# Kernel tuning notes

Hardware: AMD Instinct MI355X
Metric: run time of the kernel (lower is better)

Reference implementation:

```python
import jax, jax.numpy as jnp
import numpy as np
from jax import lax

B, C, H, W = 8, 256, 32, 32
HEADS = 8
NUM_OFF = 9
OFF_SCALE = 0.1


def setup_inputs() -> dict:
    key = jax.random.key(0)
    ks = jax.random.split(key, 8)
    f = lambda k, s, sc: jax.random.normal(k, s, dtype=jnp.float32) * sc
    return {
        'query_map': f(ks[0], (B, C, H, W), 1.0),
        'kv_map': f(ks[1], (B, C, H, W), 1.0),
        'Wq': f(ks[2], (C, C), C ** -0.5),
        'Wk': f(ks[3], (C, C), C ** -0.5),
        'Wv': f(ks[4], (C, C), C ** -0.5),
        'Woff1': f(ks[5], (C // 2, C, 3, 3), (C * 9) ** -0.5),
        'boff1': jnp.zeros((C // 2,), jnp.float32),
        'Woff2': f(ks[6], (NUM_OFF * 2, C // 2), (C // 2) ** -0.5),
        'boff2': jnp.zeros((NUM_OFF * 2,), jnp.float32),
        'Wout': f(ks[7], (C, C), C ** -0.5),
        'bout': jnp.zeros((C,), jnp.float32),
    }


def grid_sample_bilinear_border(img, grid):
    """img: (B,C,H,W); grid: (B,H,W,2) with (x,y) in [-1,1], align_corners=True,
    padding_mode='border'. Returns (B,C,H,W)."""
    Bn, Cn, Hn, Wn = img.shape
    x = (grid[..., 0] + 1.0) * 0.5 * (Wn - 1)
    y = (grid[..., 1] + 1.0) * 0.5 * (Hn - 1)
    # border padding: clamp continuous coords into the valid range
    x = jnp.clip(x, 0.0, Wn - 1)
    y = jnp.clip(y, 0.0, Hn - 1)
    x0 = jnp.floor(x)
    y0 = jnp.floor(y)
    wx = x - x0
    wy = y - y0
    x0i = x0.astype(jnp.int32)
    y0i = y0.astype(jnp.int32)
    x1i = jnp.minimum(x0i + 1, Wn - 1)
    y1i = jnp.minimum(y0i + 1, Hn - 1)
    flat = img.reshape(Bn, Cn, Hn * Wn)

    def gat(iy, ix):
        idx = (iy * Wn + ix).reshape(Bn, 1, -1)  # broadcasts over channels
        return jnp.take_along_axis(flat, idx, axis=2)

    v00 = gat(y0i, x0i)
    v01 = gat(y0i, x1i)
    v10 = gat(y1i, x0i)
    v11 = gat(y1i, x1i)
    wxf = wx.reshape(Bn, 1, -1)
    wyf = wy.reshape(Bn, 1, -1)
    out = (v00 * (1 - wxf) + v01 * wxf) * (1 - wyf) + (v10 * (1 - wxf) + v11 * wxf) * wyf
    return out.reshape(Bn, Cn, Hn, Wn)


def reference(query_map, kv_map, Wq, Wk, Wv, Woff1, boff1, Woff2, boff2, Wout, bout):
    Bn, Cn, Hn, Wn = query_map.shape
    hd = Cn // HEADS
    # 1x1 conv projections as channel einsums
    q = jnp.einsum('oc,bchw->bohw', Wq, query_map)
    # offset network: 3x3 conv -> relu -> 1x1 conv
    h1 = lax.conv_general_dilated(q, Woff1, (1, 1), 'SAME',
                                  dimension_numbers=('NCHW', 'OIHW', 'NCHW'))
    h1 = jax.nn.relu(h1 + boff1[None, :, None, None])
    offsets = jnp.einsum('oc,bchw->bohw', Woff2, h1) + boff2[None, :, None, None]
    offsets = offsets.reshape(Bn, NUM_OFF, 2, Hn, Wn)
    offset = offsets[:, 0] * OFF_SCALE  # (B,2,H,W); ch0 -> x, ch1 -> y
    # normalized base grid in [-1,1] (align_corners=True convention)
    gx = jnp.linspace(-1.0, 1.0, Wn, dtype=q.dtype)[None, :]  # (1,W)
    gy = jnp.linspace(-1.0, 1.0, Hn, dtype=q.dtype)[:, None]  # (H,1)
    vx = gx[None] + offset[:, 0]  # (B,H,W)
    vy = gy[None] + offset[:, 1]
    vgrid = jnp.stack([vx, vy], axis=-1)  # (B,H,W,2)
    kv_sampled = grid_sample_bilinear_border(kv_map, vgrid)
    k = jnp.einsum('oc,bchw->bohw', Wk, kv_sampled)
    v = jnp.einsum('oc,bchw->bohw', Wv, kv_sampled)
    # (B,C,H,W) -> (B,heads,HW,hd)
    def to_heads(t):
        return t.reshape(Bn, HEADS, hd, Hn * Wn).transpose(0, 1, 3, 2)
    qh, kh, vh = to_heads(q), to_heads(k), to_heads(v)
    scale = hd ** -0.5
    attn = jnp.einsum('bhqd,bhkd->bhqk', qh, kh) * scale
    attn = jax.nn.softmax(attn, axis=-1)
    out = jnp.einsum('bhqk,bhkd->bhqd', attn, vh)
    out = out.transpose(0, 1, 3, 2).reshape(Bn, Cn, Hn, Wn)
    out = jnp.einsum('oc,bchw->bohw', Wout, out) + bout[None, :, None, None]
    return out
```

## Files before the change

### kernel.cpp

```cpp
#include <hip/hip_runtime.h>

#define HW_ 1024

typedef __attribute__((ext_vector_type(8))) short bf16x8;
typedef __attribute__((ext_vector_type(4))) short bf16x4;
typedef __attribute__((ext_vector_type(4))) float f32x4;

__device__ inline unsigned short f2bf(float f) {
  unsigned int u = __float_as_uint(f);
  u += 0x7FFF + ((u >> 16) & 1);
  return (unsigned short)(u >> 16);
}
__device__ inline unsigned short f2bf_fast(float f) {
  return (unsigned short)((__float_as_uint(f) + 0x8000u) >> 16);
}
__device__ inline float bf2f(unsigned short h) {
  return __uint_as_float(((unsigned int)h) << 16);
}
__device__ inline void async_copy16(const void* g, void* l) {
  __builtin_amdgcn_global_load_lds(
      (const __attribute__((address_space(1))) unsigned int*)g,
      (__attribute__((address_space(3))) unsigned int*)l, 16, 0, 0);
}

__global__ __launch_bounds__(256) void fused0(
    const float* __restrict__ kv,
    const float* __restrict__ Wq, const float* __restrict__ Wk,
    const float* __restrict__ Wv, const float* __restrict__ Wo,
    const float* __restrict__ Woff1, const float* __restrict__ Xf,
    short* __restrict__ WH, short* __restrict__ WL, short* __restrict__ wb,
    float* __restrict__ kvT,
    short* __restrict__ Yt, short* __restrict__ Yh2, short* __restrict__ Yl2)
{
  __shared__ float T[256][33];
  __shared__ short Bsh[32][40];
  __shared__ short Bsl[32][40];
  const int bid = blockIdx.x, t = threadIdx.x;

  if (bid < 512) {
    const int w    = t >> 6;
    const int lane = t & 63;
    const int ln   = lane & 15;
    const int qd   = lane >> 4;
    const int bp0  = (bid & 255) * 32;
    const int om   = (bid >> 8) * 128 + w * 32;
    const int bB   = bp0 >> 10, p0l = bp0 & 1023;

    f32x4 acc[2][2] = {};
#pragma unroll
    for (int k0 = 0; k0 < 256; k0 += 32) {
      __syncthreads();
      {
        int pp = t & 31, cg = t >> 5;
        float fv[4];
#pragma unroll
        for (int j = 0; j < 4; ++j)
          fv[j] = Xf[((size_t)(bB * 256 + k0 + cg * 4 + j)) * HW_ + p0l + pp];
        bf16x4 h4, l4;
#pragma unroll
        for (int j = 0; j < 4; ++j) {
          unsigned short h = f2bf(fv[j]);
          h4[j] = (short)h;
          l4[j] = (short)f2bf(fv[j] - bf2f(h));
        }
        *(bf16x4*)&Bsh[pp][cg * 4] = h4;
        *(bf16x4*)&Bsl[pp][cg * 4] = l4;
      }
      __syncthreads();

      bf16x8 Ah[2], Al[2], Bh[2], Bl[2];
#pragma unroll
      for (int mt = 0; mt < 2; ++mt) {
        const float* ws = &Wq[((size_t)(om + mt * 16 + ln)) * 256 + k0 + qd * 8];
        float4 fa = *(const float4*)ws;
        float4 fb = *(const float4*)(ws + 4);
        float f8[8] = {fa.x, fa.y, fa.z, fa.w, fb.x, fb.y, fb.z, fb.w};
#pragma unroll
        for (int j = 0; j < 8; ++j) {
          unsigned short h = f2bf(f8[j]);
          Ah[mt][j] = (short)h;
          Al[mt][j] = (short)f2bf(f8[j] - bf2f(h));
        }
      }
#pragma unroll
      for (int nt = 0; nt < 2; ++nt) {
        Bh[nt] = *(const bf16x8*)&Bsh[nt * 16 + ln][qd * 8];
        Bl[nt] = *(const bf16x8*)&Bsl[nt * 16 + ln][qd * 8];
      }
#pragma unroll
      for (int mt = 0; mt < 2; ++mt)
#pragma unroll
        for (int nt = 0; nt < 2; ++nt) {
          acc[mt][nt] = __builtin_amdgcn_mfma_f32_16x16x32_bf16(Ah[mt], Bh[nt], acc[mt][nt], 0, 0, 0);
          acc[mt][nt] = __builtin_amdgcn_mfma_f32_16x16x32_bf16(Ah[mt], Bl[nt], acc[mt][nt], 0, 0, 0);
          acc[mt][nt] = __builtin_amdgcn_mfma_f32_16x16x32_bf16(Al[mt], Bh[nt], acc[mt][nt], 0, 0, 0);
        }
    }

    const float sc = 0.25506063286f;
#pragma unroll
    for (int mt = 0; mt < 2; ++mt)
#pragma unroll
      for (int nt = 0; nt < 2; ++nt) {
        int bp = bp0 + nt * 16 + ln;
        int b = bp >> 10, p = bp & 1023;
#pragma unroll
        for (int i = 0; i < 4; ++i) {
          int o = om + mt * 16 + qd * 4 + i;
          int h = o >> 5, d = o & 31;
          Yt[(((size_t)(b * 8 + h)) * 1024 + p) * 32 + d] = (short)f2bf(acc[mt][nt][i] * sc);
        }
        int ob = om + mt * 16 + qd * 4;
        bf16x4 h4, l4;
#pragma unroll
        for (int i = 0; i < 4; ++i) {
          float f = acc[mt][nt][i];
          unsigned short h = f2bf(f);
          h4[i] = (short)h;
          l4[i] = (short)f2bf(f - bf2f(h));
        }
        *(bf16x4*)&Yh2[(size_t)bp * 256 + ob] = h4;
        *(bf16x4*)&Yl2[(size_t)bp * 256 + ob] = l4;
      }

  } else if (bid < 768) {
    int tb = bid - 512;
    int b = tb >> 5, p0 = (tb & 31) * 32;
    int pp = t & 31, cg = t >> 5;
#pragma unroll
    for (int i = 0; i < 32; ++i) {
      int c = cg * 32 + i;
      T[c][pp] = kv[((size_t)(b * 256 + c)) * HW_ + p0 + pp];
    }
    __syncthreads();
#pragma unroll
    for (int r = 0; r < 8; ++r) {
      int e = t + 256 * r;
      int c4 = (e & 63) * 4, pp2 = e >> 6;
      float4 v4;
      v4.x = T[c4 + 0][pp2];
      v4.y = T[c4 + 1][pp2];
      v4.z = T[c4 + 2][pp2];
      v4.w = T[c4 + 3][pp2];
      *(float4*)&kvT[((size_t)(b * 1024 + p0 + pp2)) * 256 + c4] = v4;
    }
  } else if (bid < 960) {
    int b2 = bid - 768;
    int mat = b2 >> 6;
    int loc = (b2 & 63) * 1024 + t * 4;
    const float* W = (mat == 0) ? Wk : (mat == 1) ? Wv : Wo;
    float4 f4 = *(const float4*)&W[loc];
    float f[4] = {f4.x, f4.y, f4.z, f4.w};
    bf16x4 h4, l4;
#pragma unroll
    for (int j = 0; j < 4; ++j) {
      unsigned short h = f2bf(f[j]);
      h4[j] = (short)h;
      l4[j] = (short)f2bf(f[j] - bf2f(h));
    }
    *(bf16x4*)&WH[(mat + 1) * 65536 + loc] = h4;
    *(bf16x4*)&WL[(mat + 1) * 65536 + loc] = l4;
  } else {
    int e0 = (bid - 960) * 1024 + t * 4;
#pragma unroll
    for (int j = 0; j < 4; ++j) {
      int e = e0 + j;
      int c = e & 255;
      int o = (e >> 8) & 127;
      int tap = e >> 15;
      wb[e] = (short)f2bf(Woff1[((size_t)(o * 256 + c)) * 9 + tap]);
    }
  }
}

__global__ __launch_bounds__(256) void conv3x3_off(
    const short* __restrict__ wb, const float* __restrict__ bias,
    const float* __restrict__ W2,
    const short* __restrict__ xh, const short* __restrict__ xl,
    float2* __restrict__ psum)
{
  __shared__ short Xs[2][3][34][40];
  __shared__ float red[4][32][2];
  const int id   = blockIdx.x;
  const int b    = id & 7;
  const int jj   = id >> 3;
  const int y0   = jj & 31;
  const int z    = jj >> 5;
  const int t    = threadIdx.x;
  const int w    = t >> 6;
  const int lane = t & 63;
  const int ln   = lane & 15;
  const int qd   = lane >> 4;
  const int o0   = z * 64 + w * 16;

  f32x4 acc[2] = {};

  for (int c0 = 0; c0 < 256; c0 += 32) {
    __syncthreads();
#pragma unroll
    for (int i = 0; i < 3; ++i) {
      int e   = t + 256 * i;
      int oct = e & 3;
      int x   = (e >> 2) & 31;
      int r   = (e >> 7) % 3;
      int hl  = e / 384;
      int yy  = y0 + r - 1;
      bf16x8 val = {};
      if (yy >= 0 && yy < 32) {
        const short* src = hl ? xl : xh;
        val = *(const bf16x8*)&src[((size_t)((b * 32 + yy) * 32 + x)) * 256 + c0 + oct * 8];
      }
      *(bf16x8*)&Xs[hl][r][x + 1][oct * 8] = val;
    }
    if (t < 48) {
      int oct = t & 3;
      int col = ((t >> 2) & 1) ? 33 : 0;
      int r   = (t >> 3) % 3;
      int hl  = t / 24;
      bf16x8 zz = {};
      *(bf16x8*)&Xs[hl][r][col][oct * 8] = zz;
    }
    __syncthreads();

#pragma unroll
    for (int tap = 0; tap < 9; ++tap) {
      const int ky = tap / 3, kx = tap % 3;
      bf16x8 afr = *(const bf16x8*)&wb[((size_t)(tap * 128 + o0 + ln)) * 256
                                       + c0 + qd * 8];
#pragma unroll
      for (int nt = 0; nt < 2; ++nt) {
        int hc = nt * 16 + ln + kx;
        bf16x8 bh = *(const bf16x8*)&Xs[0][ky][hc][qd * 8];
        bf16x8 bl = *(const bf16x8*)&Xs[1][ky][hc][qd * 8];
        acc[nt] = __builtin_amdgcn_mfma_f32_16x16x32_bf16(afr, bh, acc[nt], 0, 0, 0);
        acc[nt] = __builtin_amdgcn_mfma_f32_16x16x32_bf16(afr, bl, acc[nt], 0, 0, 0);
      }
    }
  }

  float ps0[2] = {0.f, 0.f}, ps1[2] = {0.f, 0.f};
#pragma unroll
  for (int i = 0; i < 4; ++i) {
    int o = o0 + qd * 4 + i;
    float bo = bias[o];
    float w2a = W2[o], w2b = W2[128 + o];
#pragma unroll
    for (int nt = 0; nt < 2; ++nt) {
      float h = fmaxf(acc[nt][i] + bo, 0.f);
      ps0[nt] += w2a * h;
      ps1[nt] += w2b * h;
    }
  }
#pragma unroll
  for (int msk = 16; msk < 64; msk <<= 1) {
    ps0[0] += __shfl_xor(ps0[0], msk, 64);
    ps0[1] += __shfl_xor(ps0[1], msk, 64);
    ps1[0] += __shfl_xor(ps1[0], msk, 64);
    ps1[1] += __shfl_xor(ps1[1], msk, 64);
  }
  if (qd == 0) {
#pragma unroll
    for (int nt = 0; nt < 2; ++nt) {
      red[w][nt * 16 + ln][0] = ps0[nt];
      red[w][nt * 16 + ln][1] = ps1[nt];
    }
  }
  __syncthreads();
  if (t < 32) {
    float s0 = red[0][t][0] + red[1][t][0] + red[2][t][0] + red[3][t][0];
    float s1 = red[0][t][1] + red[1][t][1] + red[2][t][1] + red[3][t][1];
    psum[z * 8192 + (b * 32 + y0) * 32 + t] = make_float2(s0, s1);
  }
}

__global__ __launch_bounds__(512) void gemm_kv(
    const short* __restrict__ WH, const short* __restrict__ WL,
    const float* __restrict__ kvT, const float2* __restrict__ psum,
    const float* __restrict__ b2,
    short* __restrict__ kt, short* __restrict__ vt)
{
  __shared__ short XsH[32][264];
  __shared__ short XsL[32][264];
  __shared__ float2 crd[32];
  const int id  = blockIdx.x;
  const int bx  = (id & 7) * 32 + (id >> 3);
  const int bp0 = bx * 32;
  const int b   = bp0 >> 10;
  const int t   = threadIdx.x;

  if (t < 32) {
    int rowg = bp0 + t;
    float2 pA = psum[rowg];
    float2 pB = psum[8192 + rowg];
    float s0 = (pA.x + pB.x) + b2[0];
    float s1 = (pA.y + pB.y) + b2[1];
    int pix = rowg & 1023, x = pix & 31, y = pix >> 5;
    float gx = -1.f + 2.f * (float)x / 31.f;
    float gy = -1.f + 2.f * (float)y / 31.f;
    float vx = gx + 0.1f * s0;
    float vy = gy + 0.1f * s1;
    float px = fminf(fmaxf((vx + 1.f) * 0.5f * 31.f, 0.f), 31.f);
    float py = fminf(fmaxf((vy + 1.f) * 0.5f * 31.f, 0.f), 31.f);
    crd[t] = make_float2(px, py);
  }
  __syncthreads();

#pragma unroll
  for (int it = 0; it < 2; ++it) {
    int e = t + 512 * it;
    int oct = e & 31, row = e >> 5;
    float2 cd = crd[row];
    float x0f = floorf(cd.x), y0f = floorf(cd.y);
    float wx = cd.x - x0f, wy = cd.y - y0f;
    int x0 = (int)x0f, y0 = (int)y0f;
    int x1 = min(x0 + 1, 31), y1 = min(y0 + 1, 31);
    float w00 = (1.f - wx) * (1.f - wy), w01 = wx * (1.f - wy);
    float w10 = (1.f - wx) * wy,         w11 = wx * wy;
    const float* r00 = &kvT[((size_t)(b * 1024 + y0 * 32 + x0)) * 256 + oct * 8];
    const float* r01 = &kvT[((size_t)(b * 1024 + y0 * 32 + x1)) * 256 + oct * 8];
    const float* r10 = &kvT[((size_t)(b * 1024 + y1 * 32 + x0)) * 256 + oct * 8];
    const float* r11 = &kvT[((size_t)(b * 1024 + y1 * 32 + x1)) * 256 + oct * 8];
    float4 a00 = *(const float4*)r00, b00 = *(const float4*)(r00 + 4);
    float4 a01 = *(const float4*)r01, b01 = *(const float4*)(r01 + 4);
    float4 a10 = *(const float4*)r10, b10 = *(const float4*)(r10 + 4);
    float4 a11 = *(const float4*)r11, b11 = *(const float4*)(r11 + 4);
    float v[8];
    v[0] = a00.x * w00 + a01.x * w01 + a10.x * w10 + a11.x * w11;
    v[1] = a00.y * w00 + a01.y * w01 + a10.y * w10 + a11.y * w11;
    v[2] = a00.z * w00 + a01.z * w01 + a10.z * w10 + a11.z * w11;
    v[3] = a00.w * w00 + a01.w * w01 + a10.w * w10 + a11.w * w11;
    v[4] = b00.x * w00 + b01.x * w01 + b10.x * w10 + b11.x * w11;
    v[5] = b00.y * w00 + b01.y * w01 + b10.y * w10 + b11.y * w11;
    v[6] = b00.z * w00 + b01.z * w01 + b10.z * w10 + b11.z * w11;
    v[7] = b00.w * w00 + b01.w * w01 + b10.w * w10 + b11.w * w11;
    bf16x8 h8, l8;
#pragma unroll
    for (int j = 0; j < 8; ++j) {
      unsigned short h = f2bf(v[j]);
      h8[j] = (short)h;
      l8[j] = (short)f2bf(v[j] - bf2f(h));
    }
    *(bf16x8*)&XsH[row][oct * 8] = h8;
    *(bf16x8*)&XsL[row][oct * 8] = l8;
  }
  __syncthreads();

  const int w    = t >> 6;
  const int lane = t & 63;
  const int ln   = lane & 15;
  const int qd   = lane >> 4;
  const int mat  = w >> 2;
  const short* WAh = WH + (mat ? 131072 : 65536);
  const short* WAl = WL + (mat ? 131072 : 65536);
  const int om = (w & 3) * 64;

  f32x4 acc[4][2] = {};
#pragma unroll
  for (int k0 = 0; k0 < 256; k0 += 32) {
    bf16x8 Bh[2], Bl[2];
#pragma unroll
    for (int nt = 0; nt < 2; ++nt) {
      Bh[nt] = *(const bf16x8*)&XsH[nt * 16 + ln][k0 + qd * 8];
      Bl[nt] = *(const bf16x8*)&XsL[nt * 16 + ln][k0 + qd * 8];
    }
#pragma unroll
    for (int mt = 0; mt < 4; ++mt) {
      size_t wi = ((size_t)(om + mt * 16 + ln)) * 256 + k0 + qd * 8;
      bf16x8 Ah = *(const bf16x8*)&WAh[wi];
      bf16x8 Al = *(const bf16x8*)&WAl[wi];
#pragma unroll
      for (int nt = 0; nt < 2; ++nt) {
        acc[mt][nt] = __builtin_amdgcn_mfma_f32_16x16x32_bf16(Ah, Bh[nt], acc[mt][nt], 0, 0, 0);
        acc[mt][nt] = __builtin_amdgcn_mfma_f32_16x16x32_bf16(Ah, Bl[nt], acc[mt][nt], 0, 0, 0);
        acc[mt][nt] = __builtin_amdgcn_mfma_f32_16x16x32_bf16(Al, Bh[nt], acc[mt][nt], 0, 0, 0);
      }
    }
  }

#pragma unroll
  for (int mt = 0; mt < 4; ++mt)
#pragma unroll
    for (int nt = 0; nt < 2; ++nt) {
      int p  = bp0 + nt * 16 + ln;
      int pl = p & 1023;
      int jt = pl >> 6, jl = pl & 63;
#pragma unroll
      for (int i = 0; i < 4; ++i) {
        int oc = om + mt * 16 + qd * 4 + i;
        unsigned short val = f2bf(acc[mt][nt][i]);
        int bhead = b * 8 + (oc >> 5), d = oc & 31;
        if (mat == 0) {
          int cd2 = (d >> 3) ^ ((jl >> 2) & 3);
          kt[((((size_t)(bhead * 16 + jt)) * 64 + jl) * 4 + cd2) * 8 + (d & 7)] = (short)val;
        } else {
          int jjs = ((jl & 15) << 2) | (jl >> 4);
          int cj = (jjs >> 3) ^ (d & 7);
          vt[((((size_t)(bhead * 16 + jt)) * 32 + d) * 8 + cj) * 8 + (jjs & 7)] = (short)val;
        }
      }
    }
}

__global__ __launch_bounds__(256) void attn_mfma(
    const short* __restrict__ qt, const short* __restrict__ kt,
    const short* __restrict__ vt, short* __restrict__ aoh,
    short* __restrict__ aol)
{
  __shared__ __align__(16) short Ks[2][2048];
  __shared__ __align__(16) short Vs[2][2048];
  __shared__ __align__(16) short P[4][16][72];
  const int t    = threadIdx.x;
  const int w    = t >> 6;
  const int lane = t & 63;
  const int ln   = lane & 15;
  const int qd   = lane >> 4;
  const int id   = blockIdx.x;
  const int xk   = id & 7;
  const int j    = id >> 3;
  const int bh   = xk * 8 + (j >> 4);
  const int q0   = (j & 15) * 64 + w * 16;

  const short* ktb = kt + (size_t)bh * 32768;
  const short* vtb = vt + (size_t)bh * 32768;

  bf16x8 aq = *(const bf16x8*)&qt[((size_t)(bh * 1024 + q0 + ln)) * 32 + qd * 8];

  f32x4 acc[2] = {};
  float lacc[4] = {};
  const f32x4 zero = {0.f, 0.f, 0.f, 0.f};

  const int stoff = w * 512 + lane * 8;
  const int ldoff = w * 512;

  async_copy16(&ktb[stoff], &Ks[0][ldoff]);
  async_copy16(&vtb[stoff], &Vs[0][ldoff]);
  __syncthreads();

  for (int jt = 0; jt < 16; ++jt) {
    const int cur = jt & 1, nxt = cur ^ 1;
    if (jt < 15) {
      async_copy16(&ktb[(jt + 1) * 2048 + stoff], &Ks[nxt][ldoff]);
      async_copy16(&vtb[(jt + 1) * 2048 + stoff], &Vs[nxt][ldoff]);
    }

    bf16x8 bk[4], bv[2][2];
#pragma unroll
    for (int kk = 0; kk < 4; ++kk)
      bk[kk] = *(const bf16x8*)&Ks[cur][((kk * 16 + ln) * 4 + (qd ^ ((ln >> 2) & 3))) * 8];
#pragma unroll
    for (int kc = 0; kc < 2; ++kc)
#pragma unroll
      for (int ds = 0; ds < 2; ++ds)
        bv[kc][ds] = *(const bf16x8*)&Vs[cur][((ds * 16 + ln) * 8 + ((kc * 4 + qd) ^ (ln & 7))) * 8];

    f32x4 s[4];
#pragma unroll
    for (int kk = 0; kk < 4; ++kk)
      s[kk] = __builtin_amdgcn_mfma_f32_16x16x32_bf16(aq, bk[kk], zero, 0, 0, 0);

#pragma unroll
    for (int i = 0; i < 4; ++i) {
      float p0 = __builtin_amdgcn_exp2f(s[0][i]);
      float p1 = __builtin_amdgcn_exp2f(s[1][i]);
      float p2 = __builtin_amdgcn_exp2f(s[2][i]);
      float p3 = __builtin_amdgcn_exp2f(s[3][i]);
      s[0][i] = p0; s[1][i] = p1; s[2][i] = p2; s[3][i] = p3;
      lacc[i] += (p0 + p1) + (p2 + p3);
    }
#pragma unroll
    for (int i = 0; i < 4; ++i) {
      bf16x4 p4;
#pragma unroll
      for (int kk = 0; kk < 4; ++kk) p4[kk] = (short)f2bf_fast(s[kk][i]);
      *(bf16x4*)&P[w][qd * 4 + i][4 * ln] = p4;
    }
#pragma unroll
    for (int kc = 0; kc < 2; ++kc) {
      bf16x8 ap = *(const bf16x8*)&P[w][ln][kc * 32 + qd * 8];
#pragma unroll
      for (int ds = 0; ds < 2; ++ds)
        acc[ds] = __builtin_amdgcn_mfma_f32_16x16x32_bf16(ap, bv[kc][ds], acc[ds], 0, 0, 0);
    }

    __syncthreads();
  }

  const int b = bh >> 3, h = bh & 7;
#pragma unroll
  for (int i = 0; i < 4; ++i) {
    float l = lacc[i];
    l += __shfl_xor(l, 1, 64);
    l += __shfl_xor(l, 2, 64);
    l += __shfl_xor(l, 4, 64);
    l += __shfl_xor(l, 8, 64);
    float inv = 1.f / l;
    int qrow = q0 + qd * 4 + i;
#pragma unroll
    for (int ds = 0; ds < 2; ++ds) {
      float v = acc[ds][i] * inv;
      unsigned short hh = f2bf(v);
      size_t idx = ((size_t)(b * 1024 + qrow)) * 256 + h * 32 + ds * 16 + ln;
      aoh[idx] = (short)hh;
      aol[idx] = (short)f2bf(v - bf2f(hh));
    }
  }
}

__global__ __launch_bounds__(256) void gemm_out(
    const short* __restrict__ Wh, const short* __restrict__ Wl,
    const short* __restrict__ Xh, const short* __restrict__ Xl,
    const float* __restrict__ bias, float* __restrict__ Yf)
{
  const int t    = threadIdx.x;
  const int w    = t >> 6;
  const int lane = t & 63;
  const int ln   = lane & 15;
  const int qd   = lane >> 4;
  const int bp0  = blockIdx.x * 32;
  const int om   = blockIdx.y * 128 + w * 32;

  f32x4 acc[2][2] = {};
#pragma unroll
  for (int k0 = 0; k0 < 256; k0 += 32) {
    bf16x8 Ah[2], Al[2], Bh[2], Bl[2];
#pragma unroll
    for (int mt = 0; mt < 2; ++mt) {
      size_t wi = ((size_t)(om + mt * 16 + ln)) * 256 + k0 + qd * 8;
      Ah[mt] = *(const bf16x8*)&Wh[wi];
      Al[mt] = *(const bf16x8*)&Wl[wi];
    }
#pragma unroll
    for (int nt = 0; nt < 2; ++nt) {
      size_t xi = ((size_t)(bp0 + nt * 16 + ln)) * 256 + k0 + qd * 8;
      Bh[nt] = *(const bf16x8*)&Xh[xi];
      Bl[nt] = *(const bf16x8*)&Xl[xi];
    }
#pragma unroll
    for (int mt = 0; mt < 2; ++mt)
#pragma unroll
      for (int nt = 0; nt < 2; ++nt) {
        acc[mt][nt] = __builtin_amdgcn_mfma_f32_16x16x32_bf16(Ah[mt], Bh[nt], acc[mt][nt], 0, 0, 0);
        acc[mt][nt] = __builtin_amdgcn_mfma_f32_16x16x32_bf16(Ah[mt], Bl[nt], acc[mt][nt], 0, 0, 0);
        acc[mt][nt] = __builtin_amdgcn_mfma_f32_16x16x32_bf16(Al[mt], Bh[nt], acc[mt][nt], 0, 0, 0);
      }
  }

#pragma unroll
  for (int mt = 0; mt < 2; ++mt)
#pragma unroll
    for (int i = 0; i < 4; ++i) {
      int o = om + mt * 16 + qd * 4 + i;
      float bo = bias[o];
#pragma unroll
      for (int nt = 0; nt < 2; ++nt) {
        int bp = bp0 + nt * 16 + ln;
        int b = bp >> 10, p = bp & 1023;
        Yf[((size_t)(b * 256 + o)) * HW_ + p] = acc[mt][nt][i] + bo;
      }
    }
}

extern "C" void kernel_launch(void* const* d_in, const int* in_sizes, int n_in,
                              void* d_out, int out_size, void* d_ws, size_t ws_size,
                              hipStream_t stream)
{
  const float* query_map = (const float*)d_in[0];
  const float* kv_map    = (const float*)d_in[1];
  const float* Wq        = (const float*)d_in[2];
  const float* Wk        = (const float*)d_in[3];
  const float* Wv        = (const float*)d_in[4];
  const float* Woff1     = (const float*)d_in[5];
  const float* boff1     = (const float*)d_in[6];
  const float* Woff2     = (const float*)d_in[7];
  const float* boff2     = (const float*)d_in[8];
  const float* Wout      = (const float*)d_in[9];
  const float* bout      = (const float*)d_in[10];
  float* out = (float*)d_out;
  char* base = (char*)d_ws;

  const size_t MB = 1u << 20;
  float2* psum  = (float2*)(base);
  short* qt     = (short*)(base + 1 * MB);
  short* kt     = (short*)(base + 5 * MB);
  short* vt     = (short*)(base + 9 * MB);
  short* bufBh  = (short*)(base + 13 * MB);
  short* bufBl  = (short*)(base + 17 * MB);
  short* wb     = (short*)(base + 21 * MB);
  short* WH     = (short*)(base + 22 * MB);
  short* WL     = (short*)(base + 23 * MB);
  float* kvT    = (float*)(base + 24 * MB);

  dim3 blk(256);
  fused0<<<dim3(1248), blk, 0, stream>>>(kv_map, Wq, Wk, Wv, Wout, Woff1,
                                         query_map, WH, WL, wb, kvT,
                                         qt, bufBh, bufBl);
  conv3x3_off<<<dim3(512), blk, 0, stream>>>(wb, boff1, Woff2,
                                             bufBh, bufBl, psum);
  gemm_kv<<<dim3(256), dim3(512), 0, stream>>>(WH, WL, kvT, psum, boff2, kt, vt);
  attn_mfma<<<dim3(1024), blk, 0, stream>>>(qt, kt, vt, bufBh, bufBl);
  gemm_out<<<dim3(256, 2), blk, 0, stream>>>(WH + 196608, WL + 196608,
                                             bufBh, bufBl, bout, out);
}
```

Before: 181.7 us.

## Fuse offset conv into KV sampling GEMM and double query rows per attention wave

Merges the 3x3 offset convolution and the grid-sample plus K/V projection into one 512-thread kernel per image row. The offsets are reduced in shared memory and used directly, so the psum round trip and one launch go away. The attention kernel now has each wave handle two 16-row query fragments against the same K/V tiles, halving the grid and reusing loaded K/V. It also sets MFMA priority hints around the matrix phases. The costs are fewer blocks in the fused kernel (256 instead of 512 for the conv part), higher register and LDS pressure, and less parallelism in attention.

```diff
diff --git a/kernel.cpp b/kernel.cpp
--- a/kernel.cpp
+++ b/kernel.cpp
@@ -173,44 +173,49 @@
   }
 }
 
-__global__ __launch_bounds__(256) void conv3x3_off(
+__global__ __launch_bounds__(512) void convkv(
     const short* __restrict__ wb, const float* __restrict__ bias,
-    const float* __restrict__ W2,
+    const float* __restrict__ W2, const float* __restrict__ b2,
     const short* __restrict__ xh, const short* __restrict__ xl,
-    float2* __restrict__ psum)
+    const float* __restrict__ kvT,
+    const short* __restrict__ WH, const short* __restrict__ WL,
+    short* __restrict__ kt, short* __restrict__ vt)
 {
   __shared__ short Xs[2][3][34][40];
-  __shared__ float red[4][32][2];
+  __shared__ float red[8][32][2];
+  __shared__ short XsH[32][264];
+  __shared__ short XsL[32][264];
+  __shared__ float2 crd[32];
   const int id   = blockIdx.x;
   const int b    = id & 7;
-  const int jj   = id >> 3;
-  const int y0   = jj & 31;
-  const int z    = jj >> 5;
+  const int y0   = id >> 3;
   const int t    = threadIdx.x;
   const int w    = t >> 6;
   const int lane = t & 63;
   const int ln   = lane & 15;
   const int qd   = lane >> 4;
-  const int o0   = z * 64 + w * 16;
+  const int o0   = w * 16;
+  const int bp0  = (b * 32 + y0) * 32;
 
   f32x4 acc[2] = {};
-
   for (int c0 = 0; c0 < 256; c0 += 32) {
     __syncthreads();
 #pragma unroll
-    for (int i = 0; i < 3; ++i) {
-      int e   = t + 256 * i;
-      int oct = e & 3;
-      int x   = (e >> 2) & 31;
-      int r   = (e >> 7) % 3;
-      int hl  = e / 384;
-      int yy  = y0 + r - 1;
-      bf16x8 val = {};
-      if (yy >= 0 && yy < 32) {
-        const short* src = hl ? xl : xh;
-        val = *(const bf16x8*)&src[((size_t)((b * 32 + yy) * 32 + x)) * 256 + c0 + oct * 8];
-      }
-      *(bf16x8*)&Xs[hl][r][x + 1][oct * 8] = val;
+    for (int i = 0; i < 2; ++i) {
+      int e = t + 512 * i;
+      if (e < 768) {
+        int oct = e & 3;
+        int x   = (e >> 2) & 31;
+        int r   = (e >> 7) % 3;
+        int hl  = e / 384;
+        int yy  = y0 + r - 1;
+        bf16x8 val = {};
+        if (yy >= 0 && yy < 32) {
+          const short* src = hl ? xl : xh;
+          val = *(const bf16x8*)&src[((size_t)((b * 32 + yy) * 32 + x)) * 256 + c0 + oct * 8];
+        }
+        *(bf16x8*)&Xs[hl][r][x + 1][oct * 8] = val;
+      }
     }
     if (t < 48) {
       int oct = t & 3;
@@ -238,67 +243,47 @@
     }
   }
 
-  float ps0[2] = {0.f, 0.f}, ps1[2] = {0.f, 0.f};
-#pragma unroll
-  for (int i = 0; i < 4; ++i) {
-    int o = o0 + qd * 4 + i;
-    float bo = bias[o];
-    float w2a = W2[o], w2b = W2[128 + o];
-#pragma unroll
-    for (int nt = 0; nt < 2; ++nt) {
-      float h = fmaxf(acc[nt][i] + bo, 0.f);
-      ps0[nt] += w2a * h;
-      ps1[nt] += w2b * h;
-    }
-  }
-#pragma unroll
-  for (int msk = 16; msk < 64; msk <<= 1) {
-    ps0[0] += __shfl_xor(ps0[0], msk, 64);
-    ps0[1] += __shfl_xor(ps0[1], msk, 64);
-    ps1[0] += __shfl_xor(ps1[0], msk, 64);
-    ps1[1] += __shfl_xor(ps1[1], msk, 64);
-  }
-  if (qd == 0) {
-#pragma unroll
-    for (int nt = 0; nt < 2; ++nt) {
-      red[w][nt * 16 + ln][0] = ps0[nt];
-      red[w][nt * 16 + ln][1] = ps1[nt];
+  {
+    float ps0[2] = {0.f, 0.f}, ps1[2] = {0.f, 0.f};
+#pragma unroll
+    for (int i = 0; i < 4; ++i) {
+      int o = o0 + qd * 4 + i;
+      float bo = bias[o];
+      float w2a = W2[o], w2b = W2[128 + o];
+#pragma unroll
+      for (int nt = 0; nt < 2; ++nt) {
+        float h = fmaxf(acc[nt][i] + bo, 0.f);
+        ps0[nt] += w2a * h;
+        ps1[nt] += w2b * h;
+      }
+    }
+#pragma unroll
+    for (int msk = 16; msk < 64; msk <<= 1) {
+      ps0[0] += __shfl_xor(ps0[0], msk, 64);
+      ps0[1] += __shfl_xor(ps0[1], msk, 64);
+      ps1[0] += __shfl_xor(ps1[0], msk, 64);
+      ps1[1] += __shfl_xor(ps1[1], msk, 64);
+    }
+    if (qd == 0) {
+#pragma unroll
+      for (int nt = 0; nt < 2; ++nt) {
+        red[w][nt * 16 + ln][0] = ps0[nt];
+        red[w][nt * 16 + ln][1] = ps1[nt];
+      }
     }
   }
   __syncthreads();
   if (t < 32) {
-    float s0 = red[0][t][0] + red[1][t][0] + red[2][t][0] + red[3][t][0];
-    float s1 = red[0][t][1] + red[1][t][1] + red[2][t][1] + red[3][t][1];
-    psum[z * 8192 + (b * 32 + y0) * 32 + t] = make_float2(s0, s1);
-  }
-}
-
-__global__ __launch_bounds__(512) void gemm_kv(
-    const short* __restrict__ WH, const short* __restrict__ WL,
-    const float* __restrict__ kvT, const float2* __restrict__ psum,
-    const float* __restrict__ b2,
-    short* __restrict__ kt, short* __restrict__ vt)
-{
-  __shared__ short XsH[32][264];
-  __shared__ short XsL[32][264];
-  __shared__ float2 crd[32];
-  const int id  = blockIdx.x;
-  const int bx  = (id & 7) * 32 + (id >> 3);
-  const int bp0 = bx * 32;
-  const int b   = bp0 >> 10;
-  const int t   = threadIdx.x;
-
-  if (t < 32) {
-    int rowg = bp0 + t;
-    float2 pA = psum[rowg];
-    float2 pB = psum[8192 + rowg];
-    float s0 = (pA.x + pB.x) + b2[0];
-    float s1 = (pA.y + pB.y) + b2[1];
-    int pix = rowg & 1023, x = pix & 31, y = pix >> 5;
-    float gx = -1.f + 2.f * (float)x / 31.f;
-    float gy = -1.f + 2.f * (float)y / 31.f;
-    float vx = gx + 0.1f * s0;
-    float vy = gy + 0.1f * s1;
+    float a0 = red[0][t][0] + red[1][t][0] + red[2][t][0] + red[3][t][0];
+    float a1 = red[4][t][0] + red[5][t][0] + red[6][t][0] + red[7][t][0];
+    float c0s = (a0 + a1) + b2[0];
+    float d0 = red[0][t][1] + red[1][t][1] + red[2][t][1] + red[3][t][1];
+    float d1 = red[4][t][1] + red[5][t][1] + red[6][t][1] + red[7][t][1];
+    float c1s = (d0 + d1) + b2[1];
+    float gx = -1.f + 2.f * (float)t / 31.f;
+    float gy = -1.f + 2.f * (float)y0 / 31.f;
+    float vx = gx + 0.1f * c0s;
+    float vy = gy + 0.1f * c1s;
     float px = fminf(fmaxf((vx + 1.f) * 0.5f * 31.f, 0.f), 31.f);
     float py = fminf(fmaxf((vy + 1.f) * 0.5f * 31.f, 0.f), 31.f);
     crd[t] = make_float2(px, py);
@@ -312,12 +297,12 @@
     float2 cd = crd[row];
     float x0f = floorf(cd.x), y0f = floorf(cd.y);
     float wx = cd.x - x0f, wy = cd.y - y0f;
-    int x0 = (int)x0f, y0 = (int)y0f;
-    int x1 = min(x0 + 1, 31), y1 = min(y0 + 1, 31);
+    int x0 = (int)x0f, y0i = (int)y0f;
+    int x1 = min(x0 + 1, 31), y1 = min(y0i + 1, 31);
     float w00 = (1.f - wx) * (1.f - wy), w01 = wx * (1.f - wy);
     float w10 = (1.f - wx) * wy,         w11 = wx * wy;
-    const float* r00 = &kvT[((size_t)(b * 1024 + y0 * 32 + x0)) * 256 + oct * 8];
-    const float* r01 = &kvT[((size_t)(b * 1024 + y0 * 32 + x1)) * 256 + oct * 8];
+    const float* r00 = &kvT[((size_t)(b * 1024 + y0i * 32 + x0)) * 256 + oct * 8];
+    const float* r01 = &kvT[((size_t)(b * 1024 + y0i * 32 + x1)) * 256 + oct * 8];
     const float* r10 = &kvT[((size_t)(b * 1024 + y1 * 32 + x0)) * 256 + oct * 8];
     const float* r11 = &kvT[((size_t)(b * 1024 + y1 * 32 + x1)) * 256 + oct * 8];
     float4 a00 = *(const float4*)r00, b00 = *(const float4*)(r00 + 4);
@@ -345,16 +330,12 @@
   }
   __syncthreads();
 
-  const int w    = t >> 6;
-  const int lane = t & 63;
-  const int ln   = lane & 15;
-  const int qd   = lane >> 4;
   const int mat  = w >> 2;
   const short* WAh = WH + (mat ? 131072 : 65536);
   const short* WAl = WL + (mat ? 131072 : 65536);
   const int om = (w & 3) * 64;
 
-  f32x4 acc[4][2] = {};
+  f32x4 acg[4][2] = {};
 #pragma unroll
   for (int k0 = 0; k0 < 256; k0 += 32) {
     bf16x8 Bh[2], Bl[2];
@@ -370,9 +351,9 @@
       bf16x8 Al = *(const bf16x8*)&WAl[wi];
 #pragma unroll
       for (int nt = 0; nt < 2; ++nt) {
-        acc[mt][nt] = __builtin_amdgcn_mfma_f32_16x16x32_bf16(Ah, Bh[nt], acc[mt][nt], 0, 0, 0);
-        acc[mt][nt] = __builtin_amdgcn_mfma_f32_16x16x32_bf16(Ah, Bl[nt], acc[mt][nt], 0, 0, 0);
-        acc[mt][nt] = __builtin_amdgcn_mfma_f32_16x16x32_bf16(Al, Bh[nt], acc[mt][nt], 0, 0, 0);
+        acg[mt][nt] = __builtin_amdgcn_mfma_f32_16x16x32_bf16(Ah, Bh[nt], acg[mt][nt], 0, 0, 0);
+        acg[mt][nt] = __builtin_amdgcn_mfma_f32_16x16x32_bf16(Ah, Bl[nt], acg[mt][nt], 0, 0, 0);
+        acg[mt][nt] = __builtin_amdgcn_mfma_f32_16x16x32_bf16(Al, Bh[nt], acg[mt][nt], 0, 0, 0);
       }
     }
   }
@@ -387,7 +368,7 @@
 #pragma unroll
       for (int i = 0; i < 4; ++i) {
         int oc = om + mt * 16 + qd * 4 + i;
-        unsigned short val = f2bf(acc[mt][nt][i]);
+        unsigned short val = f2bf(acg[mt][nt][i]);
         int bhead = b * 8 + (oc >> 5), d = oc & 31;
         if (mat == 0) {
           int cd2 = (d >> 3) ^ ((jl >> 2) & 3);
@@ -408,25 +389,29 @@
 {
   __shared__ __align__(16) short Ks[2][2048];
   __shared__ __align__(16) short Vs[2][2048];
-  __shared__ __align__(16) short P[4][16][72];
+  __shared__ __align__(16) short P[4][32][72];
   const int t    = threadIdx.x;
   const int w    = t >> 6;
   const int lane = t & 63;
   const int ln   = lane & 15;
   const int qd   = lane >> 4;
   const int id   = blockIdx.x;
-  const int xk   = id & 7;
-  const int j    = id >> 3;
-  const int bh   = xk * 8 + (j >> 4);
-  const int q0   = (j & 15) * 64 + w * 16;
+  const int b    = id & 7;
+  const int rem  = id >> 3;
+  const int h    = rem & 7;
+  const int qc   = rem >> 3;
+  const int bh   = b * 8 + h;
+  const int qbase = qc * 128 + w * 16;
 
   const short* ktb = kt + (size_t)bh * 32768;
   const short* vtb = vt + (size_t)bh * 32768;
 
-  bf16x8 aq = *(const bf16x8*)&qt[((size_t)(bh * 1024 + q0 + ln)) * 32 + qd * 8];
-
-  f32x4 acc[2] = {};
-  float lacc[4] = {};
+  bf16x8 aq[2];
+  aq[0] = *(const bf16x8*)&qt[((size_t)(bh * 1024 + qbase + ln)) * 32 + qd * 8];
+  aq[1] = *(const bf16x8*)&qt[((size_t)(bh * 1024 + qbase + 64 + ln)) * 32 + qd * 8];
+
+  f32x4 acc[2][2] = {};
+  float lacc[2][4] = {};
   const f32x4 zero = {0.f, 0.f, 0.f, 0.f};
 
   const int stoff = w * 512 + lane * 8;
@@ -453,57 +438,66 @@
       for (int ds = 0; ds < 2; ++ds)
         bv[kc][ds] = *(const bf16x8*)&Vs[cur][((ds * 16 + ln) * 8 + ((kc * 4 + qd) ^ (ln & 7))) * 8];
 
-    f32x4 s[4];
-#pragma unroll
-    for (int kk = 0; kk < 4; ++kk)
-      s[kk] = __builtin_amdgcn_mfma_f32_16x16x32_bf16(aq, bk[kk], zero, 0, 0, 0);
-
+#pragma unroll
+    for (int qf = 0; qf < 2; ++qf) {
+      f32x4 s[4];
+      __builtin_amdgcn_s_setprio(1);
+#pragma unroll
+      for (int kk = 0; kk < 4; ++kk)
+        s[kk] = __builtin_amdgcn_mfma_f32_16x16x32_bf16(aq[qf], bk[kk], zero, 0, 0, 0);
+      __builtin_amdgcn_s_setprio(0);
+
+#pragma unroll
+      for (int i = 0; i < 4; ++i) {
+        float p0 = __builtin_amdgcn_exp2f(s[0][i]);
+        float p1 = __builtin_amdgcn_exp2f(s[1][i]);
+        float p2 = __builtin_amdgcn_exp2f(s[2][i]);
+        float p3 = __builtin_amdgcn_exp2f(s[3][i]);
+        s[0][i] = p0; s[1][i] = p1; s[2][i] = p2; s[3][i] = p3;
+        lacc[qf][i] += (p0 + p1) + (p2 + p3);
+      }
+#pragma unroll
+      for (int i = 0; i < 4; ++i) {
+        bf16x4 p4;
+#pragma unroll
+        for (int kk = 0; kk < 4; ++kk) p4[kk] = (short)f2bf_fast(s[kk][i]);
+        *(bf16x4*)&P[w][qf * 16 + qd * 4 + i][4 * ln] = p4;
+      }
+      __builtin_amdgcn_s_setprio(1);
+#pragma unroll
+      for (int kc = 0; kc < 2; ++kc) {
+        bf16x8 ap = *(const bf16x8*)&P[w][qf * 16 + ln][kc * 32 + qd * 8];
+#pragma unroll
+        for (int ds = 0; ds < 2; ++ds)
+          acc[qf][ds] = __builtin_amdgcn_mfma_f32_16x16x32_bf16(ap, bv[kc][ds], acc[qf][ds], 0, 0, 0);
+      }
+      __builtin_amdgcn_s_setprio(0);
+    }
+
+    __syncthreads();
+  }
+
+  const int bb = bh >> 3, hh2 = bh & 7;
+#pragma unroll
+  for (int qf = 0; qf < 2; ++qf)
 #pragma unroll
     for (int i = 0; i < 4; ++i) {
-      float p0 = __builtin_amdgcn_exp2f(s[0][i]);
-      float p1 = __builtin_amdgcn_exp2f(s[1][i]);
-      float p2 = __builtin_amdgcn_exp2f(s[2][i]);
-      float p3 = __builtin_amdgcn_exp2f(s[3][i]);
-      s[0][i] = p0; s[1][i] = p1; s[2][i] = p2; s[3][i] = p3;
-      lacc[i] += (p0 + p1) + (p2 + p3);
-    }
-#pragma unroll
-    for (int i = 0; i < 4; ++i) {
-      bf16x4 p4;
-#pragma unroll
-      for (int kk = 0; kk < 4; ++kk) p4[kk] = (short)f2bf_fast(s[kk][i]);
-      *(bf16x4*)&P[w][qd * 4 + i][4 * ln] = p4;
-    }
-#pragma unroll
-    for (int kc = 0; kc < 2; ++kc) {
-      bf16x8 ap = *(const bf16x8*)&P[w][ln][kc * 32 + qd * 8];
-#pragma unroll
-      for (int ds = 0; ds < 2; ++ds)
-        acc[ds] = __builtin_amdgcn_mfma_f32_16x16x32_bf16(ap, bv[kc][ds], acc[ds], 0, 0, 0);
-    }
-
-    __syncthreads();
-  }
-
-  const int b = bh >> 3, h = bh & 7;
-#pragma unroll
-  for (int i = 0; i < 4; ++i) {
-    float l = lacc[i];
-    l += __shfl_xor(l, 1, 64);
-    l += __shfl_xor(l, 2, 64);
-    l += __shfl_xor(l, 4, 64);
-    l += __shfl_xor(l, 8, 64);
-    float inv = 1.f / l;
-    int qrow = q0 + qd * 4 + i;
-#pragma unroll
-    for (int ds = 0; ds < 2; ++ds) {
-      float v = acc[ds][i] * inv;
-      unsigned short hh = f2bf(v);
-      size_t idx = ((size_t)(b * 1024 + qrow)) * 256 + h * 32 + ds * 16 + ln;
-      aoh[idx] = (short)hh;
-      aol[idx] = (short)f2bf(v - bf2f(hh));
-    }
-  }
+      float l = lacc[qf][i];
+      l += __shfl_xor(l, 1, 64);
+      l += __shfl_xor(l, 2, 64);
+      l += __shfl_xor(l, 4, 64);
+      l += __shfl_xor(l, 8, 64);
+      float inv = 1.f / l;
+      int qrow = qbase + qf * 64 + qd * 4 + i;
+#pragma unroll
+      for (int ds = 0; ds < 2; ++ds) {
+        float v = acc[qf][ds][i] * inv;
+        unsigned short hv = f2bf(v);
+        size_t idx = ((size_t)(bb * 1024 + qrow)) * 256 + hh2 * 32 + ds * 16 + ln;
+        aoh[idx] = (short)hv;
+        aol[idx] = (short)f2bf(v - bf2f(hv));
+      }
+    }
 }
 
 __global__ __launch_bounds__(256) void gemm_out(
@@ -579,7 +573,6 @@
   char* base = (char*)d_ws;
 
   const size_t MB = 1u << 20;
-  float2* psum  = (float2*)(base);
   short* qt     = (short*)(base + 1 * MB);
   short* kt     = (short*)(base + 5 * MB);
   short* vt     = (short*)(base + 9 * MB);
@@ -590,14 +583,12 @@
   short* WL     = (short*)(base + 23 * MB);
   float* kvT    = (float*)(base + 24 * MB);
 
-  dim3 blk(256);
-  fused0<<<dim3(1248), blk, 0, stream>>>(kv_map, Wq, Wk, Wv, Wout, Woff1,
-                                         query_map, WH, WL, wb, kvT,
-                                         qt, bufBh, bufBl);
-  conv3x3_off<<<dim3(512), blk, 0, stream>>>(wb, boff1, Woff2,
-                                             bufBh, bufBl, psum);
-  gemm_kv<<<dim3(256), dim3(512), 0, stream>>>(WH, WL, kvT, psum, boff2, kt, vt);
-  attn_mfma<<<dim3(1024), blk, 0, stream>>>(qt, kt, vt, bufBh, bufBl);
-  gemm_out<<<dim3(256, 2), blk, 0, stream>>>(WH + 196608, WL + 196608,
-                                             bufBh, bufBl, bout, out);
-}
+  fused0<<<dim3(1248), dim3(256), 0, stream>>>(kv_map, Wq, Wk, Wv, Wout, Woff1,
+                                               query_map, WH, WL, wb, kvT,
+                                               qt, bufBh, bufBl);
+  convkv<<<dim3(256), dim3(512), 0, stream>>>(wb, boff1, Woff2, boff2,
+                                              bufBh, bufBl, kvT, WH, WL, kt, vt);
+  attn_mfma<<<dim3(512), dim3(256), 0, stream>>>(qt, kt, vt, bufBh, bufBl);
+  gemm_out<<<dim3(256, 2), dim3(256), 0, stream>>>(WH + 196608, WL + 196608,
+                                                   bufBh, bufBl, bout, out);
+}
```

New measurement: 183.3 us. About the same (+0.9%).
